# Kernel tuning notes

Hardware: AMD Instinct MI355X
Metric: run time of the kernel (lower is better)

Reference implementation:

```python
import jax, jax.numpy as jnp
import numpy as np
import math

MAXL = 3
TAUS = [16, 16, 16, 16]
OUT_TAUS = [16, 16, 16, 16]
BM_CNT = 1.0
BM_EPS = 1e-5

# (l1, l2, l) triples in the kernel's triple-loop order, bucketed by output l
TRIPLES = {l: [] for l in range(MAXL + 1)}
for _l1 in range(MAXL + 1):
    for _l2 in range(_l1 + 1):
        for _l in range(_l1 - _l2, min(_l1 + _l2, MAXL) + 1):
            TRIPLES[_l].append((_l1, _l2))

MIDDLE_TAUS = [sum(TAUS[a] * TAUS[b] for (a, b) in TRIPLES[l]) for l in range(MAXL + 1)]


def _cg_coef(l1, m1, l2, m2, l, m):
    if m1 + m2 != m:
        return 0.0
    f = math.factorial
    pre = math.sqrt((2 * l + 1) * f(l1 + l2 - l) * f(l1 - l2 + l) * f(-l1 + l2 + l) / f(l1 + l2 + l + 1))
    pre *= math.sqrt(f(l + m) * f(l - m) * f(l1 - m1) * f(l1 + m1) * f(l2 - m2) * f(l2 + m2))
    s = 0.0
    for k in range(0, l1 + l2 - l + 1):
        d = [k, l1 + l2 - l - k, l1 - m1 - k, l2 + m2 - k, l - l2 + m1 + k, l - l1 - m2 + k]
        if any(x < 0 for x in d):
            continue
        den = 1.0
        for x in d:
            den *= f(x)
        s += (-1.0) ** k / den
    return pre * s


def _cg_tensor(l1, l2, l):
    t = np.zeros((2 * l1 + 1, 2 * l2 + 1, 2 * l + 1), dtype=np.float32)
    for i, m1 in enumerate(range(-l1, l1 + 1)):
        for j, m2 in enumerate(range(-l2, l2 + 1)):
            m = m1 + m2
            if -l <= m <= l:
                t[i, j, m + l] = _cg_coef(l1, m1, l2, m2, l, m)
    return t

CG = {}
for _l in range(MAXL + 1):
    for (_l1, _l2) in TRIPLES[_l]:
        CG[(_l1, _l2, _l)] = jnp.asarray(_cg_tensor(_l1, _l2, _l))

# complex-multiply contraction tensor: (a*b)[k] = a[i] b[j] CM[i,j,k]
_CM = np.zeros((2, 2, 2), dtype=np.float32)
_CM[0, 0, 0] = 1.0; _CM[1, 1, 0] = -1.0; _CM[0, 1, 1] = 1.0; _CM[1, 0, 1] = 1.0
CM = jnp.asarray(_CM)


def setup_inputs() -> dict:
    key = jax.random.key(0)
    k1, k2, k3 = jax.random.split(key, 3)
    in_len = sum(TAUS[l] * (2 * l + 1) for l in range(MAXL + 1))  # 256
    wlen = sum(OUT_TAUS[l] * MIDDLE_TAUS[l] for l in range(MAXL + 1))  # 90112
    activations = jax.random.normal(k1, (2048, in_len, 2), dtype=jnp.float32)
    W = 0.05 * jax.random.uniform(k2, (wlen, 2), dtype=jnp.float32)
    bn_stds = jax.random.uniform(k3, (sum(MIDDLE_TAUS),), dtype=jnp.float32)
    return {"activations": activations, "W": W, "bn_stds": bn_stds}


def reference(activations, W, bn_stds):
    B = activations.shape[0]
    # split input into per-l parts: [B, tau_l, 2l+1, 2]
    Fs = []
    st = 0
    for l in range(MAXL + 1):
        ln = TAUS[l] * (2 * l + 1)
        Fs.append(activations[:, st:st + ln, :].reshape(B, TAUS[l], 2 * l + 1, 2))
        st += ln
    outs = []
    w_st = 0
    s_st = 0
    for l in range(MAXL + 1):
        # Clebsch-Gordan products feeding output degree l
        mids = []
        for (l1, l2) in TRIPLES[l]:
            c = jnp.einsum('btmi,bsnj,mnp,ijk->btspk', Fs[l1], Fs[l2], CG[(l1, l2, l)], CM)
            mids.append(c.reshape(B, TAUS[l1] * TAUS[l2], 2 * l + 1, 2))
        mid = jnp.concatenate(mids, axis=1)  # [B, M_l, 2l+1, 2]
        Ml = MIDDLE_TAUS[l]
        # fused batchnorm: per-middle-channel std over batch and m, moving average update
        batch_std = jnp.sqrt(jnp.mean(jnp.sum(mid * mid, axis=-1), axis=(0, 2)))  # [M_l]
        mov = bn_stds[s_st:s_st + Ml]
        new_std = (mov * BM_CNT + batch_std) / (BM_CNT + 1.0)
        mid = mid / (new_std + BM_EPS)[None, :, None, None]
        # complex linear mix over middle channels -> out_taus[l]
        wl = jax.lax.dynamic_slice_in_dim(W, w_st, OUT_TAUS[l] * Ml, axis=0).reshape(OUT_TAUS[l], Ml, 2)
        out_l = jnp.einsum('oci,bcmj,ijk->bomk', wl, mid, CM)
        outs.append(out_l.reshape(B, OUT_TAUS[l] * (2 * l + 1), 2))
        w_st += OUT_TAUS[l] * Ml
        s_st += Ml
    return jnp.concatenate(outs, axis=1)  # [B, 256, 2]
```

## Files before the change

### kernel.cpp

```cpp
#include <hip/hip_runtime.h>
#include <math.h>

typedef __attribute__((ext_vector_type(8))) short bf16x8;
typedef __attribute__((ext_vector_type(4))) float f32x4;

constexpr double cfact(int n){ double r=1.0; for(int i=2;i<=n;++i) r*=(double)i; return r; }
constexpr double csqrt_(double x){ double g=(x>1.0)?x:1.0; for(int i=0;i<100;++i) g=0.5*(g+x/g); return g; }
constexpr double cg_coef_(int l1,int m1,int l2,int m2,int l,int m){
  double pre = csqrt_((double)(2*l+1)*cfact(l1+l2-l)*cfact(l1-l2+l)*cfact(-l1+l2+l)/cfact(l1+l2+l+1));
  pre = pre*csqrt_(cfact(l+m)*cfact(l-m)*cfact(l1-m1)*cfact(l1+m1)*cfact(l2-m2)*cfact(l2+m2));
  double s=0.0;
  for(int k=0;k<=l1+l2-l;++k){
    int d0=k,d1=l1+l2-l-k,d2=l1-m1-k,d3=l2+m2-k,d4=l-l2+m1+k,d5=l-l1-m2+k;
    if(d0<0||d1<0||d2<0||d3<0||d4<0||d5<0) continue;
    double den=cfact(d0)*cfact(d1)*cfact(d2)*cfact(d3)*cfact(d4)*cfact(d5);
    s+=((k&1)?-1.0:1.0)/den;
  }
  return pre*s;
}
struct CGList{ int n; float coef[64]; int mi[64]; int ni[64]; int pi[64]; };
constexpr CGList build_cg(int l1,int l2,int l){
  CGList T{};
  for(int i=0;i<2*l1+1;++i){
    for(int j=0;j<2*l2+1;++j){
      int m1=i-l1, m2=j-l2, m=m1+m2;
      if(m<-l||m>l) continue;
      double c=cg_coef_(l1,m1,l2,m2,l,m);
      if(c>1e-12||c<-1e-12){
        T.coef[T.n]=(float)c; T.mi[T.n]=i; T.ni[T.n]=j; T.pi[T.n]=m+l; T.n++;
      }
    }
  }
  return T;
}

__device__ __host__ constexpr int AOFF(int l){ return l==0?0: l==1?16: l==2?64:144; }
__device__ __host__ constexpr int MLs(int l){ return l==0?1024: l==1?1536: l==2?1792:1536; }
__device__ __host__ constexpr int WOFF(int l){ return l==0?0: l==1?16384: l==2?40960:69632; }
__device__ __host__ constexpr int SOFF(int l){ return l==0?0: l==1?1024: l==2?2560:4352; }
__device__ __host__ constexpr int ABASE(int l){ return l==0?0: l==1?65536: l==2?163840:278528; }

#define DEVFN __device__ __forceinline__
#define BP 68
#define AP 68

DEVFN unsigned f2bf2(float x, float y){
  unsigned ux = __float_as_uint(x); ux = (ux + 0x7FFFu + ((ux>>16)&1u)) >> 16;
  unsigned uy = __float_as_uint(y); uy = (uy + 0x7FFFu + ((uy>>16)&1u)) >> 16;
  return (ux & 0xFFFFu) | (uy << 16);
}

template<int L1,int L2,int L>
DEVFN void cg_accum(const float2* F1, const float2* F2, float2* mid){
  constexpr CGList T = build_cg(L1,L2,L);
  #pragma unroll
  for(int e=0;e<T.n;++e){
    const float c = T.coef[e];
    const float2 a = F1[T.mi[e]];
    const float2 b = F2[T.ni[e]];
    float pr = a.x*b.x - a.y*b.y;
    float pim= a.x*b.y + a.y*b.x;
    mid[T.pi[e]].x += c*pr;
    mid[T.pi[e]].y += c*pim;
  }
}

template<int L1,int L2,int L>
DEVFN void k1g(const float2* __restrict__ act2, int b0, int u, int bh,
               float& ssa, float& ssb){
  constexpr int N1=2*L1+1, N2=2*L2+1, NP=2*L+1;
  const int t = u>>3, s0 = (u&7)*2;
  const float2* base1  = act2 + AOFF(L1) + t*N1;
  const float2* base2a = act2 + AOFF(L2) + s0*N2;
  const float2* base2b = base2a + N2;
  #pragma unroll 2
  for(int bi=0;bi<16;++bi){
    const size_t ro = (size_t)(b0 + bh*16 + bi)*256;
    float2 F1[N1], F2a[N2], F2b[N2], mida[NP], midb[NP];
    #pragma unroll
    for(int m=0;m<N1;++m) F1[m]=base1[ro+m];
    #pragma unroll
    for(int n=0;n<N2;++n){ F2a[n]=base2a[ro+n]; F2b[n]=base2b[ro+n]; }
    #pragma unroll
    for(int p=0;p<NP;++p){ mida[p]=make_float2(0.f,0.f); midb[p]=make_float2(0.f,0.f); }
    cg_accum<L1,L2,L>(F1,F2a,mida);
    cg_accum<L1,L2,L>(F1,F2b,midb);
    #pragma unroll
    for(int p=0;p<NP;++p){
      ssa += mida[p].x*mida[p].x + mida[p].y*mida[p].y;
      ssb += midb[p].x*midb[p].x + midb[p].y*midb[p].y;
    }
  }
}

DEVFN void convW(const float* __restrict__ W, short* __restrict__ A, int idx){
  int l = (idx<1024)?0 : (idx<2560)?1 : (idx<4352)?2 : 3;
  int c = idx - SOFF(l);
  int Ml = MLs(l);
  const float2* wbase = (const float2*)W + WOFF(l) + c;
  unsigned* Aw = (unsigned*)(A + ABASE(l));
  #pragma unroll 4
  for(int o=0;o<16;++o){
    float2 w = wbase[(size_t)o*Ml];
    Aw[(size_t)o*Ml + c]      = f2bf2(w.x, -w.y);
    Aw[(size_t)(o+16)*Ml + c] = f2bf2(w.y,  w.x);
  }
}

__global__ __launch_bounds__(256) void k_sumsq(const float* __restrict__ act,
                                               float2* __restrict__ part,
                                               const float* __restrict__ W,
                                               short* __restrict__ A){
  const int bid = blockIdx.x;
  const int tid = threadIdx.x;
  if(bid >= 1472){
    convW(W, A, (bid-1472)*256 + tid);
    return;
  }
  const int order[23] = {22,16,21,18,15,20,13,9,14,8,17,7,12,6,10,3,5,19,2,11,1,4,0};
  const int ti = order[bid>>6];
  const int chunk = bid&63;
  const int b0 = chunk*32;
  const int u = tid & 127, bh = tid >> 7;
  const float2* act2 = (const float2*)act;
  float ssa=0.f, ssb=0.f;
  switch(ti){
    case 0:  k1g<0,0,0>(act2,b0,u,bh,ssa,ssb); break;
    case 1:  k1g<1,1,0>(act2,b0,u,bh,ssa,ssb); break;
    case 2:  k1g<2,2,0>(act2,b0,u,bh,ssa,ssb); break;
    case 3:  k1g<3,3,0>(act2,b0,u,bh,ssa,ssb); break;
    case 4:  k1g<1,0,1>(act2,b0,u,bh,ssa,ssb); break;
    case 5:  k1g<1,1,1>(act2,b0,u,bh,ssa,ssb); break;
    case 6:  k1g<2,1,1>(act2,b0,u,bh,ssa,ssb); break;
    case 7:  k1g<2,2,1>(act2,b0,u,bh,ssa,ssb); break;
    case 8:  k1g<3,2,1>(act2,b0,u,bh,ssa,ssb); break;
    case 9:  k1g<3,3,1>(act2,b0,u,bh,ssa,ssb); break;
    case 10: k1g<1,1,2>(act2,b0,u,bh,ssa,ssb); break;
    case 11: k1g<2,0,2>(act2,b0,u,bh,ssa,ssb); break;
    case 12: k1g<2,1,2>(act2,b0,u,bh,ssa,ssb); break;
    case 13: k1g<2,2,2>(act2,b0,u,bh,ssa,ssb); break;
    case 14: k1g<3,1,2>(act2,b0,u,bh,ssa,ssb); break;
    case 15: k1g<3,2,2>(act2,b0,u,bh,ssa,ssb); break;
    case 16: k1g<3,3,2>(act2,b0,u,bh,ssa,ssb); break;
    case 17: k1g<2,1,3>(act2,b0,u,bh,ssa,ssb); break;
    case 18: k1g<2,2,3>(act2,b0,u,bh,ssa,ssb); break;
    case 19: k1g<3,0,3>(act2,b0,u,bh,ssa,ssb); break;
    case 20: k1g<3,1,3>(act2,b0,u,bh,ssa,ssb); break;
    case 21: k1g<3,2,3>(act2,b0,u,bh,ssa,ssb); break;
    default: k1g<3,3,3>(act2,b0,u,bh,ssa,ssb); break;
  }
  part[(size_t)((ti*64 + chunk)*2 + bh)*128 + u] = make_float2(ssa, ssb);
}

__global__ __launch_bounds__(256) void k_scale(const float* __restrict__ bn,
                                               const float2* __restrict__ part,
                                               float* __restrict__ s){
  const int ti = blockIdx.x;
  const int ch = threadIdx.x;
  const int idx = ti*256 + ch;
  const int u = ch>>1;
  const float2* ps = part + (size_t)ti*128*128 + u;
  float sum = 0.f;
  #pragma unroll 8
  for(int r=0;r<128;++r){
    float2 v = ps[(size_t)r*128];
    sum += (ch&1) ? v.y : v.x;
  }
  int l = (idx<1024)?0 : (idx<2560)?1 : (idx<4352)?2 : 3;
  float divi = (l==0)?(1.f/2048.f) : (l==1)?(1.f/6144.f) : (l==2)?(1.f/10240.f) : (1.f/14336.f);
  float bstd = sqrtf(sum*divi);
  float nstd = 0.5f*(bn[idx]+bstd);
  s[idx] = 1.f/(nstd+1e-5f);
}


#define BT_B   0
#define LA_B   17408

template<int NTIL>
DEVFN void kf_pre(char* smem){
  const int tid = threadIdx.x;
  unsigned* btile = (unsigned*)(smem + BT_B);
  for(int i=tid; i<NTIL*16*BP; i+=256) btile[i]=0;
  __syncthreads();
}

template<int L1,int L2,int L,int Q,int NTIL>
DEVFN void kf_triple(const float2* __restrict__ act2, int b0, char* smem,
                     const unsigned* __restrict__ Aw,
                     const float* __restrict__ sg, f32x4& cR, f32x4& cI){
  constexpr int N1=2*L1+1, N2=2*L2+1, NP=2*L+1;
  constexpr int Ml = MLs(L);
  unsigned* btile  = (unsigned*)(smem + BT_B);
  unsigned* ldsA   = (unsigned*)(smem + LA_B);
  const int tid = threadIdx.x;
  const int lane = tid & 63, w = tid >> 6;
  const int col = lane & 15, quad = lane >> 4;
  const int up = tid & 31, bi = tid >> 5;
  const int r0 = tid>>4,       j0 = (tid&15)*4;
  const int r1 = (tid+256)>>4;
  const float2* arow = act2 + (size_t)(b0+bi)*256;
  uint4 v0 = *(const uint4*)(Aw + (size_t)r0*Ml + Q*256 + j0);
  uint4 v1 = *(const uint4*)(Aw + (size_t)r1*Ml + Q*256 + j0);
  #pragma unroll 1
  for(int cc=0; cc<4; ++cc){
    {
      const float2 s2 = *(const float2*)(sg + SOFF(L) + Q*256 + cc*64 + 2*up);
      const int u = cc*32 + up;
      const int t = u>>3, s0 = (u&7)*2;
      float2 F1[N1], F2a[N2], F2b[N2], mida[NP], midb[NP];
      #pragma unroll
      for(int m=0;m<N1;++m) F1[m]=arow[AOFF(L1)+t*N1+m];
      #pragma unroll
      for(int n=0;n<N2;++n){
        F2a[n]=arow[AOFF(L2)+s0*N2+n];
        F2b[n]=arow[AOFF(L2)+(s0+1)*N2+n];
      }
      #pragma unroll
      for(int p=0;p<NP;++p){ mida[p]=make_float2(0.f,0.f); midb[p]=make_float2(0.f,0.f); }
      cg_accum<L1,L2,L>(F1,F2a,mida);
      cg_accum<L1,L2,L>(F1,F2b,midb);
      #pragma unroll
      for(int p=0;p<NP;++p){
        uint2 v;
        v.x = f2bf2(mida[p].x*s2.x, mida[p].y*s2.x);
        v.y = f2bf2(midb[p].x*s2.y, midb[p].y*s2.y);
        *(uint2*)(btile + (size_t)(bi*NP+p)*BP + 2*up) = v;
      }
    }
    *(uint4*)(ldsA + r0*AP + j0) = v0;
    *(uint4*)(ldsA + r1*AP + j0) = v1;
    if(cc<3){
      const int base = Q*256 + (cc+1)*64;
      v0 = *(const uint4*)(Aw + (size_t)r0*Ml + base + j0);
      v1 = *(const uint4*)(Aw + (size_t)r1*Ml + base + j0);
    }
    __syncthreads();
    if(w < NTIL){
      const unsigned* ar0 = ldsA + col*AP + quad*4;
      const unsigned* ar1 = ldsA + (col+16)*AP + quad*4;
      const unsigned* bb  = btile + (w*16+col)*BP + quad*4;
      #pragma unroll
      for(int ks=0; ks<4; ++ks){
        bf16x8 b  = *(const bf16x8*)(bb + ks*16);
        bf16x8 A0 = *(const bf16x8*)(ar0 + ks*16);
        bf16x8 A1 = *(const bf16x8*)(ar1 + ks*16);
        cR = __builtin_amdgcn_mfma_f32_16x16x32_bf16(A0, b, cR, 0, 0, 0);
        cI = __builtin_amdgcn_mfma_f32_16x16x32_bf16(A1, b, cI, 0, 0, 0);
      }
    }
    __syncthreads();
  }
}

template<int L,int NTIL>
DEVFN void kf_epi(float* __restrict__ out, int b0, f32x4 cR, f32x4 cI){
  constexpr int NP = 2*L+1;
  const int tid = threadIdx.x, lane = tid & 63, w = tid >> 6;
  const int col = lane & 15, quad = lane >> 4;
  if(w < NTIL){
    const int r = w*16 + col;
    if(r < 8*NP){
      const int b = b0 + r/NP, p = r - (r/NP)*NP;
      float2* o2 = (float2*)out + (size_t)b*256 + AOFF(L);
      #pragma unroll
      for(int i=0;i<4;++i) o2[(quad*4+i)*NP + p] = make_float2(cR[i], cI[i]);
    }
  }
}

__global__ __launch_bounds__(256,3) void k_fusedall(const float* __restrict__ act,
    const short* __restrict__ A, const float* __restrict__ sg,
    float* __restrict__ out){
  __shared__ __align__(16) char smem[26112];
  const int bid = blockIdx.x;
  const float2* act2 = (const float2*)act;
  f32x4 cR={0.f,0.f,0.f,0.f}, cI={0.f,0.f,0.f,0.f};
  if(bid < 256){
    const int b0 = bid*8;
    kf_pre<4>(smem);
    const unsigned* Aw=(const unsigned*)(A+ABASE(3));
    kf_triple<2,1,3,0,4>(act2,b0,smem,Aw,sg,cR,cI);
    kf_triple<2,2,3,1,4>(act2,b0,smem,Aw,sg,cR,cI);
    kf_triple<3,0,3,2,4>(act2,b0,smem,Aw,sg,cR,cI);
    kf_triple<3,1,3,3,4>(act2,b0,smem,Aw,sg,cR,cI);
    kf_triple<3,2,3,4,4>(act2,b0,smem,Aw,sg,cR,cI);
    kf_triple<3,3,3,5,4>(act2,b0,smem,Aw,sg,cR,cI);
    kf_epi<3,4>(out,b0,cR,cI);
  } else if(bid < 512){
    const int b0 = (bid-256)*8;
    kf_pre<3>(smem);
    const unsigned* Aw=(const unsigned*)(A+ABASE(2));
    kf_triple<1,1,2,0,3>(act2,b0,smem,Aw,sg,cR,cI);
    kf_triple<2,0,2,1,3>(act2,b0,smem,Aw,sg,cR,cI);
    kf_triple<2,1,2,2,3>(act2,b0,smem,Aw,sg,cR,cI);
    kf_triple<2,2,2,3,3>(act2,b0,smem,Aw,sg,cR,cI);
    kf_triple<3,1,2,4,3>(act2,b0,smem,Aw,sg,cR,cI);
    kf_triple<3,2,2,5,3>(act2,b0,smem,Aw,sg,cR,cI);
    kf_triple<3,3,2,6,3>(act2,b0,smem,Aw,sg,cR,cI);
    kf_epi<2,3>(out,b0,cR,cI);
  } else if(bid < 768){
    const int b0 = (bid-512)*8;
    kf_pre<2>(smem);
    const unsigned* Aw=(const unsigned*)(A+ABASE(1));
    kf_triple<1,0,1,0,2>(act2,b0,smem,Aw,sg,cR,cI);
    kf_triple<1,1,1,1,2>(act2,b0,smem,Aw,sg,cR,cI);
    kf_triple<2,1,1,2,2>(act2,b0,smem,Aw,sg,cR,cI);
    kf_triple<2,2,1,3,2>(act2,b0,smem,Aw,sg,cR,cI);
    kf_triple<3,2,1,4,2>(act2,b0,smem,Aw,sg,cR,cI);
    kf_triple<3,3,1,5,2>(act2,b0,smem,Aw,sg,cR,cI);
    kf_epi<1,2>(out,b0,cR,cI);
  } else {
    const int b0 = (bid-768)*8;
    kf_pre<1>(smem);
    const unsigned* Aw=(const unsigned*)(A+ABASE(0));
    kf_triple<0,0,0,0,1>(act2,b0,smem,Aw,sg,cR,cI);
    kf_triple<1,1,0,1,1>(act2,b0,smem,Aw,sg,cR,cI);
    kf_triple<2,2,0,2,1>(act2,b0,smem,Aw,sg,cR,cI);
    kf_triple<3,3,0,3,1>(act2,b0,smem,Aw,sg,cR,cI);
    kf_epi<0,1>(out,b0,cR,cI);
  }
}

extern "C" void kernel_launch(void* const* d_in, const int* in_sizes, int n_in,
                              void* d_out, int out_size, void* d_ws, size_t ws_size,
                              hipStream_t stream) {
  const float* act = (const float*)d_in[0];
  const float* W   = (const float*)d_in[1];
  const float* bn  = (const float*)d_in[2];
  float* out = (float*)d_out;

  float*  s    = (float*)d_ws;
  short*  A    = (short*)((char*)d_ws + 24576);
  float2* part = (float2*)((char*)d_ws + 1048576);

  hipLaunchKernelGGL(k_sumsq,   dim3(1495), dim3(256), 0, stream, act, part, W, A);
  hipLaunchKernelGGL(k_scale,   dim3(23),   dim3(256), 0, stream, bn, part, s);
  hipLaunchKernelGGL(k_fusedall,dim3(1024), dim3(256), 0, stream, act, A, s, out);
}
```

Before: 142.8 us.

## Double-buffer LDS tiles to overlap CG product compute with MFMA mixing

Splits the shared-memory B tile and A weight tile into two ping-pong buffers, so each chunk's Clebsch-Gordan products and weight stores for the next chunk are produced while MFMAs consume the current chunk. This halves the barriers per chunk loop, from two to one, and prefetches weights two chunks ahead. In exchange, LDS per block doubles (about 51 KB), which may limit the three-blocks-per-CU occupancy target. It also adds barriers between triples and widens the zero-fill.

```diff
diff --git a/kernel.cpp b/kernel.cpp
--- a/kernel.cpp
+++ b/kernel.cpp
@@ -174,16 +174,11 @@
 }
 
 
-#define BT_B   0
-#define LA_B   17408
-
-template<int NTIL>
-DEVFN void kf_pre(char* smem){
-  const int tid = threadIdx.x;
-  unsigned* btile = (unsigned*)(smem + BT_B);
-  for(int i=tid; i<NTIL*16*BP; i+=256) btile[i]=0;
-  __syncthreads();
-}
+#define BT0_W 0
+#define BTS_W 4352
+#define LA0_W 8704
+#define LAS_W 2176
+#define SM_SZ 52224
 
 template<int L1,int L2,int L,int Q,int NTIL>
 DEVFN void kf_triple(const float2* __restrict__ act2, int b0, char* smem,
@@ -191,55 +186,70 @@
                      const float* __restrict__ sg, f32x4& cR, f32x4& cI){
   constexpr int N1=2*L1+1, N2=2*L2+1, NP=2*L+1;
   constexpr int Ml = MLs(L);
-  unsigned* btile  = (unsigned*)(smem + BT_B);
-  unsigned* ldsA   = (unsigned*)(smem + LA_B);
+  unsigned* lds = (unsigned*)smem;
   const int tid = threadIdx.x;
   const int lane = tid & 63, w = tid >> 6;
   const int col = lane & 15, quad = lane >> 4;
   const int up = tid & 31, bi = tid >> 5;
-  const int r0 = tid>>4,       j0 = (tid&15)*4;
-  const int r1 = (tid+256)>>4;
+  const int r0 = tid>>4, j0 = (tid&15)*4, r1 = (tid+256)>>4;
   const float2* arow = act2 + (size_t)(b0+bi)*256;
+
+  auto phase1 = [&](int ccx){
+    unsigned* btile = lds + BT0_W + (ccx&1)*BTS_W;
+    const float2 s2 = *(const float2*)(sg + SOFF(L) + Q*256 + ccx*64 + 2*up);
+    const int u = ccx*32 + up;
+    const int t = u>>3, s0 = (u&7)*2;
+    float2 F1[N1], F2a[N2], F2b[N2], mida[NP], midb[NP];
+    #pragma unroll
+    for(int m=0;m<N1;++m) F1[m]=arow[AOFF(L1)+t*N1+m];
+    #pragma unroll
+    for(int n=0;n<N2;++n){
+      F2a[n]=arow[AOFF(L2)+s0*N2+n];
+      F2b[n]=arow[AOFF(L2)+(s0+1)*N2+n];
+    }
+    #pragma unroll
+    for(int p=0;p<NP;++p){ mida[p]=make_float2(0.f,0.f); midb[p]=make_float2(0.f,0.f); }
+    cg_accum<L1,L2,L>(F1,F2a,mida);
+    cg_accum<L1,L2,L>(F1,F2b,midb);
+    #pragma unroll
+    for(int p=0;p<NP;++p){
+      uint2 v;
+      v.x = f2bf2(mida[p].x*s2.x, mida[p].y*s2.x);
+      v.y = f2bf2(midb[p].x*s2.y, midb[p].y*s2.y);
+      *(uint2*)(btile + (size_t)(bi*NP+p)*BP + 2*up) = v;
+    }
+  };
+
   uint4 v0 = *(const uint4*)(Aw + (size_t)r0*Ml + Q*256 + j0);
   uint4 v1 = *(const uint4*)(Aw + (size_t)r1*Ml + Q*256 + j0);
+  phase1(0);
+  {
+    unsigned* lac = lds + LA0_W;
+    *(uint4*)(lac + r0*AP + j0) = v0;
+    *(uint4*)(lac + r1*AP + j0) = v1;
+  }
+  v0 = *(const uint4*)(Aw + (size_t)r0*Ml + Q*256 + 64 + j0);
+  v1 = *(const uint4*)(Aw + (size_t)r1*Ml + Q*256 + 64 + j0);
+  __syncthreads();
   #pragma unroll 1
   for(int cc=0; cc<4; ++cc){
-    {
-      const float2 s2 = *(const float2*)(sg + SOFF(L) + Q*256 + cc*64 + 2*up);
-      const int u = cc*32 + up;
-      const int t = u>>3, s0 = (u&7)*2;
-      float2 F1[N1], F2a[N2], F2b[N2], mida[NP], midb[NP];
-      #pragma unroll
-      for(int m=0;m<N1;++m) F1[m]=arow[AOFF(L1)+t*N1+m];
-      #pragma unroll
-      for(int n=0;n<N2;++n){
-        F2a[n]=arow[AOFF(L2)+s0*N2+n];
-        F2b[n]=arow[AOFF(L2)+(s0+1)*N2+n];
+    if(cc<3){
+      phase1(cc+1);
+      unsigned* lac = lds + LA0_W + ((cc+1)&1)*LAS_W;
+      *(uint4*)(lac + r0*AP + j0) = v0;
+      *(uint4*)(lac + r1*AP + j0) = v1;
+      if(cc<2){
+        const int base = Q*256 + (cc+2)*64;
+        v0 = *(const uint4*)(Aw + (size_t)r0*Ml + base + j0);
+        v1 = *(const uint4*)(Aw + (size_t)r1*Ml + base + j0);
       }
-      #pragma unroll
-      for(int p=0;p<NP;++p){ mida[p]=make_float2(0.f,0.f); midb[p]=make_float2(0.f,0.f); }
-      cg_accum<L1,L2,L>(F1,F2a,mida);
-      cg_accum<L1,L2,L>(F1,F2b,midb);
-      #pragma unroll
-      for(int p=0;p<NP;++p){
-        uint2 v;
-        v.x = f2bf2(mida[p].x*s2.x, mida[p].y*s2.x);
-        v.y = f2bf2(midb[p].x*s2.y, midb[p].y*s2.y);
-        *(uint2*)(btile + (size_t)(bi*NP+p)*BP + 2*up) = v;
-      }
-    }
-    *(uint4*)(ldsA + r0*AP + j0) = v0;
-    *(uint4*)(ldsA + r1*AP + j0) = v1;
-    if(cc<3){
-      const int base = Q*256 + (cc+1)*64;
-      v0 = *(const uint4*)(Aw + (size_t)r0*Ml + base + j0);
-      v1 = *(const uint4*)(Aw + (size_t)r1*Ml + base + j0);
-    }
-    __syncthreads();
+    }
     if(w < NTIL){
-      const unsigned* ar0 = ldsA + col*AP + quad*4;
-      const unsigned* ar1 = ldsA + (col+16)*AP + quad*4;
-      const unsigned* bb  = btile + (w*16+col)*BP + quad*4;
+      const unsigned* lac = lds + LA0_W + (cc&1)*LAS_W;
+      const unsigned* btc = lds + BT0_W + (cc&1)*BTS_W;
+      const unsigned* ar0 = lac + col*AP + quad*4;
+      const unsigned* ar1 = lac + (col+16)*AP + quad*4;
+      const unsigned* bb  = btc + (w*16+col)*BP + quad*4;
       #pragma unroll
       for(int ks=0; ks<4; ++ks){
         bf16x8 b  = *(const bf16x8*)(bb + ks*16);
@@ -249,8 +259,15 @@
         cI = __builtin_amdgcn_mfma_f32_16x16x32_bf16(A1, b, cI, 0, 0, 0);
       }
     }
-    __syncthreads();
-  }
+    if(cc<3) __syncthreads();
+  }
+}
+
+DEVFN void kf_pre(char* smem){
+  const int tid = threadIdx.x;
+  unsigned* lds = (unsigned*)smem;
+  for(int i=tid; i<2*BTS_W; i+=256) lds[i]=0;
+  __syncthreads();
 }
 
 template<int L,int NTIL>
@@ -272,51 +289,70 @@
 __global__ __launch_bounds__(256,3) void k_fusedall(const float* __restrict__ act,
     const short* __restrict__ A, const float* __restrict__ sg,
     float* __restrict__ out){
-  __shared__ __align__(16) char smem[26112];
+  __shared__ __align__(16) char smem[SM_SZ];
   const int bid = blockIdx.x;
   const float2* act2 = (const float2*)act;
   f32x4 cR={0.f,0.f,0.f,0.f}, cI={0.f,0.f,0.f,0.f};
   if(bid < 256){
     const int b0 = bid*8;
-    kf_pre<4>(smem);
+    kf_pre(smem);
     const unsigned* Aw=(const unsigned*)(A+ABASE(3));
     kf_triple<2,1,3,0,4>(act2,b0,smem,Aw,sg,cR,cI);
+    __syncthreads();
     kf_triple<2,2,3,1,4>(act2,b0,smem,Aw,sg,cR,cI);
+    __syncthreads();
     kf_triple<3,0,3,2,4>(act2,b0,smem,Aw,sg,cR,cI);
+    __syncthreads();
     kf_triple<3,1,3,3,4>(act2,b0,smem,Aw,sg,cR,cI);
+    __syncthreads();
     kf_triple<3,2,3,4,4>(act2,b0,smem,Aw,sg,cR,cI);
+    __syncthreads();
     kf_triple<3,3,3,5,4>(act2,b0,smem,Aw,sg,cR,cI);
     kf_epi<3,4>(out,b0,cR,cI);
   } else if(bid < 512){
     const int b0 = (bid-256)*8;
-    kf_pre<3>(smem);
+    kf_pre(smem);
     const unsigned* Aw=(const unsigned*)(A+ABASE(2));
     kf_triple<1,1,2,0,3>(act2,b0,smem,Aw,sg,cR,cI);
+    __syncthreads();
     kf_triple<2,0,2,1,3>(act2,b0,smem,Aw,sg,cR,cI);
+    __syncthreads();
     kf_triple<2,1,2,2,3>(act2,b0,smem,Aw,sg,cR,cI);
+    __syncthreads();
     kf_triple<2,2,2,3,3>(act2,b0,smem,Aw,sg,cR,cI);
+    __syncthreads();
     kf_triple<3,1,2,4,3>(act2,b0,smem,Aw,sg,cR,cI);
+    __syncthreads();
     kf_triple<3,2,2,5,3>(act2,b0,smem,Aw,sg,cR,cI);
+    __syncthreads();
     kf_triple<3,3,2,6,3>(act2,b0,smem,Aw,sg,cR,cI);
     kf_epi<2,3>(out,b0,cR,cI);
   } else if(bid < 768){
     const int b0 = (bid-512)*8;
-    kf_pre<2>(smem);
+    kf_pre(smem);
     const unsigned* Aw=(const unsigned*)(A+ABASE(1));
     kf_triple<1,0,1,0,2>(act2,b0,smem,Aw,sg,cR,cI);
+    __syncthreads();
     kf_triple<1,1,1,1,2>(act2,b0,smem,Aw,sg,cR,cI);
+    __syncthreads();
     kf_triple<2,1,1,2,2>(act2,b0,smem,Aw,sg,cR,cI);
+    __syncthreads();
     kf_triple<2,2,1,3,2>(act2,b0,smem,Aw,sg,cR,cI);
+    __syncthreads();
     kf_triple<3,2,1,4,2>(act2,b0,smem,Aw,sg,cR,cI);
+    __syncthreads();
     kf_triple<3,3,1,5,2>(act2,b0,smem,Aw,sg,cR,cI);
     kf_epi<1,2>(out,b0,cR,cI);
   } else {
     const int b0 = (bid-768)*8;
-    kf_pre<1>(smem);
+    kf_pre(smem);
     const unsigned* Aw=(const unsigned*)(A+ABASE(0));
     kf_triple<0,0,0,0,1>(act2,b0,smem,Aw,sg,cR,cI);
+    __syncthreads();
     kf_triple<1,1,0,1,1>(act2,b0,smem,Aw,sg,cR,cI);
+    __syncthreads();
     kf_triple<2,2,0,2,1>(act2,b0,smem,Aw,sg,cR,cI);
+    __syncthreads();
     kf_triple<3,3,0,3,1>(act2,b0,smem,Aw,sg,cR,cI);
     kf_epi<0,1>(out,b0,cR,cI);
   }
```

Result: slower. 148.2 us (+3.8%).
